# Optimization experiments

Hardware: AMD Instinct MI355X
Metric: run time of the kernel (lower is better)

The kernel has to match this reference:

```python
import jax, jax.numpy as jnp
import numpy as np

B, T, C, H = 1, 1024, 2048, 32
N = C // H  # head_dim = 64
EPS_GN = 0.00064


def setup_inputs() -> dict:
    key = jax.random.key(0)
    ks = jax.random.split(key, 40)
    f32 = jnp.float32

    def rn(k, shape, s):
        return jax.random.normal(k, shape, f32) * s

    layer_idx, n_layer = 12, 24
    r01 = layer_idx / (n_layer - 1)
    r1a0 = 1.0 - layer_idx / n_layer
    ddd = (jnp.arange(C, dtype=f32) / C).reshape(1, 1, C)
    decay_speed = -7.0 + 5.0 * (jnp.arange(C, dtype=f32) / (C - 1)) ** (0.85 + r01 ** 0.5)

    inp = dict(
        hidden_states=jax.random.normal(ks[0], (B, T, C), f32),
        Wq=rn(ks[1], (C, C), 0.02), Wk=rn(ks[2], (C, C), 0.02),
        Wv=rn(ks[3], (C, C), 0.02), Wo=rn(ks[4], (C, C), 0.02),
        time_maa_x=1.0 - ddd ** (0.6 * r1a0 ** 0.9),
        time_maa_rg=rn(ks[5], (1, 1, C), 0.01),
        time_maa_wa=rn(ks[6], (1, 1, C), 0.01),
        time_maa_k=rn(ks[7], (1, 1, C), 0.01),
        time_maa_v=rn(ks[8], (1, 1, C), 0.01),
        time_maa_w1=rn(ks[9], (C, 4 * 32), 0.01),
        time_maa_w2=rn(ks[10], (4, 32, C), 0.01),
        time_decay=decay_speed.reshape(1, 1, C) + 0.5,
        time_decay_w1=rn(ks[11], (C, 64), 0.01),
        time_decay_w2=rn(ks[12], (64, C), 0.01),
        time_aaaaa=rn(ks[13], (1, 1, C), 0.01),
        time_aaa_w1=rn(ks[14], (C, 16), 0.01),
        time_aaa_w2=rn(ks[15], (16, C), 0.01),
        time_kkk_w1=rn(ks[16], (C, 16), 0.01),
        time_kkk_w2=rn(ks[17], (16, C), 0.01),
        gate_w1=rn(ks[18], (C, 128), 0.01),
        gate_w2=rn(ks[19], (128, C), 0.01),
        time_misc_a=rn(ks[20], (1, 1, C), 0.01),
        ma_w1=rn(ks[21], (C, 16), 0.01),
        ma_w2=rn(ks[22], (16, C), 0.01),
        time_misc_k=rn(ks[23], (1, 1, C), 0.01),
        mk_w1=rn(ks[24], (C, 16), 0.01),
        mk_w2=rn(ks[25], (16, C), 0.01),
        time_faaaa=rn(ks[26], (1, 1, H, N), 0.01),
        ln_w=1.0 + rn(ks[27], (C,), 0.01),
        ln_b=rn(ks[28], (C,), 0.01),
    )
    return inp


def _wkv7(r, w, k, v, a, b):
    """RWKV7 matrix-state recurrence. Inputs [B,T,C]; per head state [N,N].
    state_t = state * exp(w_t) (per key-col) + (state @ a_t) b_t^T + v_t k_t^T;
    out_t = state_t @ r_t."""
    hs = lambda x: x.reshape(B, T, H, N)
    r, k, v, a, b = map(hs, (r, k, v, a, b))
    dec = jnp.exp(hs(w))  # w <= -0.5, decay in (0,1)

    def step(state, inp):
        r_t, d_t, k_t, v_t, a_t, b_t = inp  # each [B,H,N]
        sa = jnp.einsum('bhij,bhj->bhi', state, a_t)
        state = (state * d_t[:, :, None, :]
                 + sa[..., None] * b_t[:, :, None, :]
                 + v_t[..., None] * k_t[:, :, None, :])
        out = jnp.einsum('bhij,bhj->bhi', state, r_t)
        return state, out

    xs = tuple(jnp.moveaxis(t, 1, 0) for t in (r, dec, k, v, a, b))  # [T,B,H,N]
    state0 = jnp.zeros((B, H, N, N), r.dtype)
    _, out = jax.lax.scan(step, state0, xs)
    return jnp.moveaxis(out, 0, 1).reshape(B, T, C)


def _group_norm(x, w, b):
    xg = x.reshape(B, T, H, N)
    mu = xg.mean(-1, keepdims=True)
    var = xg.var(-1, keepdims=True)
    xn = (xg - mu) * jax.lax.rsqrt(var + EPS_GN)
    return xn.reshape(B, T, C) * w + b


def reference(hidden_states, Wq, Wk, Wv, Wo, time_maa_x, time_maa_rg, time_maa_wa,
              time_maa_k, time_maa_v, time_maa_w1, time_maa_w2, time_decay,
              time_decay_w1, time_decay_w2, time_aaaaa, time_aaa_w1, time_aaa_w2,
              time_kkk_w1, time_kkk_w2, gate_w1, gate_w2, time_misc_a, ma_w1, ma_w2,
              time_misc_k, mk_w1, mk_w2, time_faaaa, ln_w, ln_b):
    x = hidden_states  # T already multiple of 16, so no padding branch
    dxprev = jnp.pad(x, ((0, 0), (1, 0), (0, 0)))[:, :-1] - x  # token shift
    xxx = x + dxprev * time_maa_x
    mix = jnp.tanh(xxx @ time_maa_w1).reshape(B, T, 4, 32)
    mix = jnp.einsum('btfd,fdc->fbtc', mix, time_maa_w2)  # [4,B,T,C]
    mrg, mwa, mk_mix, mv = mix[0], mix[1], mix[2], mix[3]
    xrg = x + dxprev * (time_maa_rg + mrg)
    xwa = x + dxprev * (time_maa_wa + mwa)
    xk = x + dxprev * (time_maa_k + mk_mix)
    xv = x + dxprev * (time_maa_v + mv)

    r = xrg @ Wq
    w = -jax.nn.softplus(-(time_decay + jnp.tanh(xwa @ time_decay_w1) @ time_decay_w2)) - 0.5
    k = xk @ Wk
    v = xv @ Wv
    g = jnp.tanh(xrg @ gate_w1) @ gate_w2

    kk = k + jnp.tanh(xk @ time_kkk_w1) @ time_kkk_w2
    kkh = kk.reshape(B, T, H, N)
    kk = (kkh / jnp.maximum(jnp.linalg.norm(kkh, axis=-1, keepdims=True), 1e-12)).reshape(B, T, C)

    a = jax.nn.sigmoid(time_aaaaa + (xwa @ time_aaa_w1) @ time_aaa_w2)
    ma = jax.nn.sigmoid(time_misc_a + (xwa @ ma_w1) @ ma_w2)
    k = k * ma + k * a * (1.0 - ma)
    mk_g = jax.nn.sigmoid(time_misc_k + (xk @ mk_w1) @ mk_w2)
    k = k * jnp.exp(jnp.minimum(w * mk_g, 0.0))

    y = _wkv7(r, w, k, v, -kk, kk * a)
    y = _group_norm(y, ln_w, ln_b)
    rh, kh, vh = (t.reshape(B, T, H, N) for t in (r, k, v))
    y = y + ((rh * kh * time_faaaa).sum(-1, keepdims=True) * vh).reshape(B, T, C)
    return (y * g) @ Wo
```

## Files before the change

kernel.cpp:

```cpp
#include <hip/hip_runtime.h>


#define T_ 1024
#define C_ 2048
#define H_ 32
#define N_ 64

using half8  = __attribute__((ext_vector_type(8))) _Float16;
using half4  = __attribute__((ext_vector_type(4))) _Float16;
using floatx4 = __attribute__((ext_vector_type(4))) float;

#define DPP_ADD(v, ctrl) \
    ((v) + __int_as_float(__builtin_amdgcn_update_dpp( \
        0, __float_as_int(v), (ctrl), 0xf, 0xf, true)))
#define REDUCE16(v) do { \
    v = DPP_ADD(v, 0xB1); v = DPP_ADD(v, 0x4E); \
    v = DPP_ADD(v, 0x141); v = DPP_ADD(v, 0x140); } while (0)

__global__ __launch_bounds__(256) void k_tr(
    const float* __restrict__ W0, const float* __restrict__ W1,
    const float* __restrict__ W2, const float* __restrict__ W3,
    _Float16* __restrict__ D0, _Float16* __restrict__ D1,
    _Float16* __restrict__ D2, _Float16* __restrict__ D3)
{
    const int z = blockIdx.z;
    const float* S = (z == 0) ? W0 : (z == 1) ? W1 : (z == 2) ? W2 : W3;
    _Float16* D = (z == 0) ? D0 : (z == 1) ? D1 : (z == 2) ? D2 : D3;
    const int nb = blockIdx.x * 64, kb = blockIdx.y * 64;
    __shared__ __align__(16) float tile[64][65];
    const int tr = threadIdx.x >> 4, tc4 = (threadIdx.x & 15) * 4;
#pragma unroll
    for (int p = 0; p < 4; ++p) {
        int row = p * 16 + tr;
        float4 v = *(const float4*)&S[(size_t)(kb + row) * C_ + nb + tc4];
        tile[row][tc4 + 0] = v.x; tile[row][tc4 + 1] = v.y;
        tile[row][tc4 + 2] = v.z; tile[row][tc4 + 3] = v.w;
    }
    __syncthreads();
#pragma unroll
    for (int p = 0; p < 4; ++p) {
        int n = p * 16 + tr;
        half4 u;
        u[0] = (_Float16)tile[tc4 + 0][n];
        u[1] = (_Float16)tile[tc4 + 1][n];
        u[2] = (_Float16)tile[tc4 + 2][n];
        u[3] = (_Float16)tile[tc4 + 3][n];
        *(half4*)&D[(size_t)(nb + n) * C_ + kb + tc4] = u;
    }
}

__global__ __launch_bounds__(256) void k_trW(
    const float* __restrict__ maa_w1, const float* __restrict__ gate_w1,
    const float* __restrict__ decay_w1, const float* __restrict__ aaa_w1,
    const float* __restrict__ ma_w1, const float* __restrict__ kkk_w1,
    const float* __restrict__ mk_w1,
    _Float16* __restrict__ WTm, _Float16* __restrict__ WTl)
{
    const int z = blockIdx.z;
    const int k = blockIdx.x * 256 + threadIdx.x;
    const int n = blockIdx.y;
    if (z == 0 && n >= 128) return;
    const float* src; int stride, col;
    _Float16* dst;
    if (z == 0) { src = maa_w1; stride = 128; col = n; dst = WTm; }
    else {
        dst = WTl;
        if (n < 128)      { src = gate_w1;  stride = 128; col = n; }
        else if (n < 192) { src = decay_w1; stride = 64;  col = n - 128; }
        else if (n < 208) { src = aaa_w1;   stride = 16;  col = n - 192; }
        else if (n < 224) { src = ma_w1;    stride = 16;  col = n - 208; }
        else if (n < 240) { src = kkk_w1;   stride = 16;  col = n - 224; }
        else              { src = mk_w1;    stride = 16;  col = n - 240; }
    }
    dst[(size_t)n * C_ + k] = (_Float16)src[(size_t)k * stride + col];
}

__global__ __launch_bounds__(256) void k_prep(
    const float* __restrict__ X, const float* __restrict__ maa_x,
    _Float16* __restrict__ xxxH)
{
    const size_t idx = (size_t)blockIdx.x * 256 + threadIdx.x;
    const int c = (int)(idx & (C_ - 1));
    float cur = X[idx];
    float prev = (idx >= C_) ? X[idx - C_] : 0.0f;
    xxxH[idx] = (_Float16)(cur + (prev - cur) * maa_x[c]);
}

__global__ __launch_bounds__(256) void k_lora(
    int which,
    const _Float16* __restrict__ Axxx, const _Float16* __restrict__ Axrg,
    const _Float16* __restrict__ Axwa, const _Float16* __restrict__ Axk,
    const _Float16* __restrict__ WTm, const _Float16* __restrict__ WTl,
    float* __restrict__ m1p, float* __restrict__ l2p)
{
    const int mt = blockIdx.x;
    const int nt = blockIdx.y;
    const int ks = blockIdx.z;
    const _Float16* A; const _Float16* BT; float* O; int ostride;
    if (which == 0) { A = Axxx; BT = WTm; O = m1p; ostride = 128; }
    else {
        BT = WTl; O = l2p; ostride = 256;
        A = (nt < 4) ? Axrg : (nt < 7) ? Axwa : Axk;
    }
    O += (size_t)ks * T_ * ostride;
    const int m0 = mt * 64, n0 = nt * 32, k0 = ks * 512;
    const int tid = threadIdx.x;
    __shared__ __align__(16) _Float16 As[64 * 40];
    __shared__ __align__(16) _Float16 Bs[32 * 40];
    const int lane = tid & 63, wv = tid >> 6;
    const int r16 = lane & 15, q = lane >> 4;

    floatx4 acc[2];
    { floatx4 zv = {0.f, 0.f, 0.f, 0.f}; acc[0] = zv; acc[1] = zv; }

    const int arow = tid >> 2, ac8 = (tid & 3) * 8;
    const _Float16* ag = A + (size_t)(m0 + arow) * C_ + k0 + ac8;
    const _Float16* bg = BT + (size_t)(n0 + (tid >> 2)) * C_ + k0 + ac8;

    for (int kc = 0; kc < 512; kc += 32) {
        half8 av = *(const half8*)(ag + kc);
        half8 bv;
        if (tid < 128) bv = *(const half8*)(bg + kc);
        *(half8*)&As[arow * 40 + ac8] = av;
        if (tid < 128) *(half8*)&Bs[(tid >> 2) * 40 + ac8] = bv;
        __syncthreads();
        half8 af = *(const half8*)&As[(wv * 16 + r16) * 40 + q * 8];
        half8 b0 = *(const half8*)&Bs[(r16) * 40 + q * 8];
        half8 b1 = *(const half8*)&Bs[(16 + r16) * 40 + q * 8];
        acc[0] = __builtin_amdgcn_mfma_f32_16x16x32_f16(af, b0, acc[0], 0, 0, 0);
        acc[1] = __builtin_amdgcn_mfma_f32_16x16x32_f16(af, b1, acc[1], 0, 0, 0);
        __syncthreads();
    }
#pragma unroll
    for (int j = 0; j < 2; ++j)
#pragma unroll
        for (int e = 0; e < 4; ++e) {
            int row = m0 + wv * 16 + q * 4 + e;
            int col = n0 + j * 16 + r16;
            O[(size_t)row * ostride + col] = acc[j][e];
        }
}

__global__ __launch_bounds__(256) void k_xmix(
    const float* __restrict__ X, const float* __restrict__ m1p,
    const float* __restrict__ w2,
    const float* __restrict__ mrg, const float* __restrict__ mwa,
    const float* __restrict__ mk, const float* __restrict__ mv,
    _Float16* __restrict__ xrgH, _Float16* __restrict__ xwaH,
    _Float16* __restrict__ xkH, _Float16* __restrict__ xvH)
{
    const int tid = threadIdx.x;
    const int c = blockIdx.x * 256 + tid;
    const int t0 = blockIdx.y * 16;
    const size_t P = (size_t)T_ * 128;
    __shared__ __align__(16) float m1s[16][128];
#pragma unroll
    for (int p = 0; p < 2; ++p) {
        int id = tid + p * 256;
        int r = id >> 5, c4 = (id & 31) * 4;
        size_t off = (size_t)(t0 + r) * 128 + c4;
        float4 v0 = *(const float4*)&m1p[off];
        float4 v1 = *(const float4*)&m1p[P + off];
        float4 v2 = *(const float4*)&m1p[2 * P + off];
        float4 v3 = *(const float4*)&m1p[3 * P + off];
        float4 v;
        v.x = tanhf(((v0.x + v1.x) + v2.x) + v3.x);
        v.y = tanhf(((v0.y + v1.y) + v2.y) + v3.y);
        v.z = tanhf(((v0.z + v1.z) + v2.z) + v3.z);
        v.w = tanhf(((v0.w + v1.w) + v2.w) + v3.w);
        *(float4*)&m1s[r][c4] = v;
    }
    __syncthreads();
    float a0[16], a1[16], a2[16], a3[16];
#pragma unroll
    for (int t = 0; t < 16; ++t) { a0[t] = 0.f; a1[t] = 0.f; a2[t] = 0.f; a3[t] = 0.f; }
    for (int d = 0; d < 32; ++d) {
        float w0 = w2[(size_t)(0 * 32 + d) * C_ + c];
        float w1 = w2[(size_t)(1 * 32 + d) * C_ + c];
        float w2v = w2[(size_t)(2 * 32 + d) * C_ + c];
        float w3 = w2[(size_t)(3 * 32 + d) * C_ + c];
#pragma unroll
        for (int t = 0; t < 16; ++t) {
            a0[t] = fmaf(m1s[t][d],      w0,  a0[t]);
            a1[t] = fmaf(m1s[t][32 + d], w1,  a1[t]);
            a2[t] = fmaf(m1s[t][64 + d], w2v, a2[t]);
            a3[t] = fmaf(m1s[t][96 + d], w3,  a3[t]);
        }
    }
    float vrg = mrg[c], vwa = mwa[c], vmk = mk[c], vmv = mv[c];
    float prev = (t0 > 0) ? X[(size_t)(t0 - 1) * C_ + c] : 0.0f;
    for (int t = 0; t < 16; ++t) {
        size_t idx = (size_t)(t0 + t) * C_ + c;
        float cur = X[idx];
        float dx = prev - cur;
        xrgH[idx] = (_Float16)(cur + dx * (vrg + a0[t]));
        xwaH[idx] = (_Float16)(cur + dx * (vwa + a1[t]));
        xkH[idx]  = (_Float16)(cur + dx * (vmk + a2[t]));
        xvH[idx]  = (_Float16)(cur + dx * (vmv + a3[t]));
        prev = cur;
    }
}

__global__ __launch_bounds__(256) void k_gemm(
    const _Float16* __restrict__ A0, const _Float16* __restrict__ B0, float* __restrict__ C0,
    const _Float16* __restrict__ A1, const _Float16* __restrict__ B1, float* __restrict__ C1,
    const _Float16* __restrict__ A2, const _Float16* __restrict__ B2, float* __restrict__ C2)
{
    const int z = blockIdx.z;
    const _Float16* A = (z == 0) ? A0 : (z == 1) ? A1 : A2;
    const _Float16* Bt = (z == 0) ? B0 : (z == 1) ? B1 : B2;
    float* C = (z == 0) ? C0 : (z == 1) ? C1 : C2;
    const int mtile = blockIdx.y * 128;
    const int ntile = blockIdx.x * 128;
    const int tid = threadIdx.x;
    __shared__ __align__(16) _Float16 As[128 * 40];
    __shared__ __align__(16) _Float16 Bs[128 * 40];
    const int lane = tid & 63;
    const int wvid = tid >> 6;
    const int wm = wvid >> 1, wn = wvid & 1;
    const int r16 = lane & 15, q = lane >> 4;

    floatx4 acc[4][4];
#pragma unroll
    for (int i = 0; i < 4; ++i)
#pragma unroll
        for (int j = 0; j < 4; ++j) { floatx4 zv = {0.f, 0.f, 0.f, 0.f}; acc[i][j] = zv; }

    const int srow = tid >> 1, shalf = tid & 1;
    const _Float16* ag = A + (size_t)(mtile + srow) * C_ + shalf * 16;
    const _Float16* bg = Bt + (size_t)(ntile + srow) * C_ + shalf * 16;
    _Float16* asw = &As[srow * 40 + shalf * 16];
    _Float16* bsw = &Bs[srow * 40 + shalf * 16];

    for (int kc = 0; kc < C_; kc += 32) {
        half8 a0 = *(const half8*)(ag + kc);
        half8 a1 = *(const half8*)(ag + kc + 8);
        half8 b0 = *(const half8*)(bg + kc);
        half8 b1 = *(const half8*)(bg + kc + 8);
        *(half8*)asw = a0; *(half8*)(asw + 8) = a1;
        *(half8*)bsw = b0; *(half8*)(bsw + 8) = b1;
        __syncthreads();

        half8 af[4], bf[4];
#pragma unroll
        for (int i = 0; i < 4; ++i)
            af[i] = *(const half8*)&As[(wm * 64 + i * 16 + r16) * 40 + q * 8];
#pragma unroll
        for (int j = 0; j < 4; ++j)
            bf[j] = *(const half8*)&Bs[(wn * 64 + j * 16 + r16) * 40 + q * 8];
#pragma unroll
        for (int i = 0; i < 4; ++i)
#pragma unroll
            for (int j = 0; j < 4; ++j)
                acc[i][j] = __builtin_amdgcn_mfma_f32_16x16x32_f16(af[i], bf[j], acc[i][j], 0, 0, 0);
        __syncthreads();
    }
#pragma unroll
    for (int i = 0; i < 4; ++i)
#pragma unroll
        for (int j = 0; j < 4; ++j)
#pragma unroll
            for (int e = 0; e < 4; ++e) {
                int row = mtile + wm * 64 + i * 16 + q * 4 + e;
                int col = ntile + wn * 64 + j * 16 + r16;
                C[(size_t)row * C_ + col] = acc[i][j][e];
            }
}

__global__ __launch_bounds__(256) void k_fuse(
    const float* __restrict__ l2p,
    float* __restrict__ K0,
    const float* __restrict__ decay_w2, const float* __restrict__ aaa_w2,
    const float* __restrict__ ma_w2, const float* __restrict__ kkk_w2,
    const float* __restrict__ mk_w2,
    const float* __restrict__ tdecay, const float* __restrict__ aaaaa,
    const float* __restrict__ misc_a, const float* __restrict__ misc_k,
    float* __restrict__ Wout, float* __restrict__ KKout, float* __restrict__ Aout)
{
    const int tid = threadIdx.x;
    const int c = blockIdx.x * 256 + tid;
    const int t0 = blockIdx.y * 16;
    const size_t P = (size_t)T_ * 256;
    __shared__ __align__(16) float wsS[16][96];
    __shared__ __align__(16) float ksS[16][32];
    for (int id = tid; id < 16 * 24; id += 256) {
        int r = id / 24, c4 = (id % 24) * 4;
        size_t off = (size_t)(t0 + r) * 256 + 128 + c4;
        float4 v0 = *(const float4*)&l2p[off];
        float4 v1 = *(const float4*)&l2p[P + off];
        float4 v2 = *(const float4*)&l2p[2 * P + off];
        float4 v3 = *(const float4*)&l2p[3 * P + off];
        float4 v;
        v.x = ((v0.x + v1.x) + v2.x) + v3.x;
        v.y = ((v0.y + v1.y) + v2.y) + v3.y;
        v.z = ((v0.z + v1.z) + v2.z) + v3.z;
        v.w = ((v0.w + v1.w) + v2.w) + v3.w;
        if (c4 < 64) { v.x = tanhf(v.x); v.y = tanhf(v.y); v.z = tanhf(v.z); v.w = tanhf(v.w); }
        *(float4*)&wsS[r][c4] = v;
    }
    for (int id = tid; id < 16 * 8; id += 256) {
        int r = id / 8, c4 = (id % 8) * 4;
        size_t off = (size_t)(t0 + r) * 256 + 224 + c4;
        float4 v0 = *(const float4*)&l2p[off];
        float4 v1 = *(const float4*)&l2p[P + off];
        float4 v2 = *(const float4*)&l2p[2 * P + off];
        float4 v3 = *(const float4*)&l2p[3 * P + off];
        float4 v;
        v.x = ((v0.x + v1.x) + v2.x) + v3.x;
        v.y = ((v0.y + v1.y) + v2.y) + v3.y;
        v.z = ((v0.z + v1.z) + v2.z) + v3.z;
        v.w = ((v0.w + v1.w) + v2.w) + v3.w;
        if (c4 < 16) { v.x = tanhf(v.x); v.y = tanhf(v.y); v.z = tanhf(v.z); v.w = tanhf(v.w); }
        *(float4*)&ksS[r][c4] = v;
    }
    __syncthreads();
    float accW[16], accA[16], accMA[16], accKK[16], accMK[16];
#pragma unroll
    for (int r = 0; r < 16; ++r) { accW[r] = 0.f; accA[r] = 0.f; accMA[r] = 0.f; accKK[r] = 0.f; accMK[r] = 0.f; }
    for (int j = 0; j < 64; ++j) {
        float w = decay_w2[(size_t)j * C_ + c];
#pragma unroll
        for (int r = 0; r < 16; ++r) accW[r] = fmaf(wsS[r][j], w, accW[r]);
    }
    for (int j = 0; j < 16; ++j) {
        float wa = aaa_w2[(size_t)j * C_ + c];
        float wm = ma_w2[(size_t)j * C_ + c];
        float wk = kkk_w2[(size_t)j * C_ + c];
        float wq = mk_w2[(size_t)j * C_ + c];
#pragma unroll
        for (int r = 0; r < 16; ++r) {
            accA[r]  = fmaf(wsS[r][64 + j], wa, accA[r]);
            accMA[r] = fmaf(wsS[r][80 + j], wm, accMA[r]);
            accKK[r] = fmaf(ksS[r][j],      wk, accKK[r]);
            accMK[r] = fmaf(ksS[r][16 + j], wq, accMK[r]);
        }
    }
    float td = tdecay[c], aa = aaaaa[c], mia = misc_a[c], mik = misc_k[c];
    for (int r = 0; r < 16; ++r) {
        size_t idx = (size_t)(t0 + r) * C_ + c;
        float wraw = td + accW[r];
        float w = -logf(1.0f + __expf(-wraw)) - 0.5f;
        float a  = 1.0f / (1.0f + __expf(-(aa  + accA[r])));
        float mav = 1.0f / (1.0f + __expf(-(mia + accMA[r])));
        float mkv = 1.0f / (1.0f + __expf(-(mik + accMK[r])));
        float k0 = K0[idx];
        Wout[idx]  = w;
        KKout[idx] = k0 + accKK[r];
        K0[idx]    = k0 * (mav + a * (1.0f - mav)) * __expf(fminf(w * mkv, 0.0f));
        Aout[idx]  = a;
    }
}

__global__ __launch_bounds__(256) void k_kknorm(float* __restrict__ KK, float* __restrict__ Ab)
{
    const int t = blockIdx.y;
    const int c = blockIdx.x * 256 + threadIdx.x;
    const size_t idx = (size_t)t * C_ + c;
    float kv = KK[idx];
    float ss = kv * kv;
    ss += __shfl_xor(ss, 1, 64);  ss += __shfl_xor(ss, 2, 64);
    ss += __shfl_xor(ss, 4, 64);  ss += __shfl_xor(ss, 8, 64);
    ss += __shfl_xor(ss, 16, 64); ss += __shfl_xor(ss, 32, 64);
    float scale = 1.0f / fmaxf(sqrtf(ss), 1e-12f);
    float kn = kv * scale;
    KK[idx] = kn;
    Ab[idx] = kn * Ab[idx];
}

__global__ __launch_bounds__(256) void k_gate2(
    const float* __restrict__ l2p, const float* __restrict__ w2, float* __restrict__ G)
{
    const int tid = threadIdx.x;
    const int c = blockIdx.x * 256 + tid;
    const int t0 = blockIdx.y * 16;
    const size_t P = (size_t)T_ * 256;
    __shared__ __align__(16) float gs[16][128];
#pragma unroll
    for (int p = 0; p < 2; ++p) {
        int id = tid + p * 256;
        int r = id >> 5, c4 = (id & 31) * 4;
        size_t off = (size_t)(t0 + r) * 256 + c4;
        float4 v0 = *(const float4*)&l2p[off];
        float4 v1 = *(const float4*)&l2p[P + off];
        float4 v2 = *(const float4*)&l2p[2 * P + off];
        float4 v3 = *(const float4*)&l2p[3 * P + off];
        float4 v;
        v.x = tanhf(((v0.x + v1.x) + v2.x) + v3.x);
        v.y = tanhf(((v0.y + v1.y) + v2.y) + v3.y);
        v.z = tanhf(((v0.z + v1.z) + v2.z) + v3.z);
        v.w = tanhf(((v0.w + v1.w) + v2.w) + v3.w);
        *(float4*)&gs[r][c4] = v;
    }
    __syncthreads();
    float acc[16];
#pragma unroll
    for (int r = 0; r < 16; ++r) acc[r] = 0.f;
    for (int j = 0; j < 128; ++j) {
        float w = w2[(size_t)j * C_ + c];
#pragma unroll
        for (int r = 0; r < 16; ++r) acc[r] = fmaf(gs[r][j], w, acc[r]);
    }
    for (int r = 0; r < 16; ++r) G[(size_t)(t0 + r) * C_ + c] = acc[r];
}

__global__ __launch_bounds__(256) void k_wkv(
    const float* __restrict__ R, const float* __restrict__ Wd,
    const float* __restrict__ K, const float* __restrict__ V,
    const float* __restrict__ KK, const float* __restrict__ Bb,
    float* __restrict__ Y)
{
    const int tid = threadIdx.x;
    const int h = blockIdx.x >> 2;
    const int rg = blockIdx.x & 3;
    const int c0 = h * 64;
    const int wv = tid >> 6, lane = tid & 63;
    const int irow = rg * 16 + wv * 4 + (lane >> 4);
    const int jg = lane & 15;
    __shared__ __align__(16) float rS[16][64], dS[16][64], kS[16][64],
                                   vS[16][64], aS[16][64], bS[16][64], oS[16][64];
    float4 s = make_float4(0.f, 0.f, 0.f, 0.f);
    const int tloc = tid >> 4, j4 = (tid & 15) * 4;

    for (int tc = 0; tc < T_; tc += 16) {
        size_t gi = (size_t)(tc + tloc) * C_ + c0 + j4;
        *(float4*)&rS[tloc][j4] = *(const float4*)&R[gi];
        float4 w4 = *(const float4*)&Wd[gi];
        float4 d4;
        d4.x = __expf(w4.x); d4.y = __expf(w4.y); d4.z = __expf(w4.z); d4.w = __expf(w4.w);
        *(float4*)&dS[tloc][j4] = d4;
        *(float4*)&kS[tloc][j4] = *(const float4*)&K[gi];
        *(float4*)&vS[tloc][j4] = *(const float4*)&V[gi];
        float4 kk4 = *(const float4*)&KK[gi];
        float4 a4 = make_float4(-kk4.x, -kk4.y, -kk4.z, -kk4.w);
        *(float4*)&aS[tloc][j4] = a4;
        *(float4*)&bS[tloc][j4] = *(const float4*)&Bb[gi];
        __syncthreads();

#pragma unroll
        for (int tt = 0; tt < 16; ++tt) {
            float4 a = *(float4*)&aS[tt][jg * 4];
            float sa = s.x * a.x + s.y * a.y + s.z * a.z + s.w * a.w;
            REDUCE16(sa);
            float vi = vS[tt][irow];
            float4 d = *(float4*)&dS[tt][jg * 4];
            float4 b = *(float4*)&bS[tt][jg * 4];
            float4 k = *(float4*)&kS[tt][jg * 4];
            s.x = fmaf(s.x, d.x, fmaf(sa, b.x, vi * k.x));
            s.y = fmaf(s.y, d.y, fmaf(sa, b.y, vi * k.y));
            s.z = fmaf(s.z, d.z, fmaf(sa, b.z, vi * k.z));
            s.w = fmaf(s.w, d.w, fmaf(sa, b.w, vi * k.w));
            float4 r = *(float4*)&rS[tt][jg * 4];
            float o = s.x * r.x + s.y * r.y + s.z * r.z + s.w * r.w;
            REDUCE16(o);
            if (jg == 0) oS[tt][irow] = o;
        }
        __syncthreads();
        Y[(size_t)(tc + tloc) * C_ + c0 + rg * 16 + (tid & 15)] = oS[tloc][rg * 16 + (tid & 15)];
    }
}

__global__ __launch_bounds__(256) void k_gn(
    const float* __restrict__ Y, const float* __restrict__ R, const float* __restrict__ K,
    const float* __restrict__ V, const float* __restrict__ G,
    const float* __restrict__ faaaa, const float* __restrict__ lnw,
    const float* __restrict__ lnb, _Float16* __restrict__ YG)
{
    const int t = blockIdx.y;
    const int c = blockIdx.x * 256 + threadIdx.x;
    const size_t idx = (size_t)t * C_ + c;
    float y = Y[idx];
    float s1 = y, s2 = y * y;
#pragma unroll
    for (int off = 1; off < 64; off <<= 1) {
        s1 += __shfl_xor(s1, off, 64);
        s2 += __shfl_xor(s2, off, 64);
    }
    float mu = s1 * (1.0f / 64.0f);
    float var = s2 * (1.0f / 64.0f) - mu * mu;
    float gn = (y - mu) * rsqrtf(var + 0.00064f) * lnw[c] + lnb[c];
    float p = R[idx] * K[idx] * faaaa[c];
#pragma unroll
    for (int off = 1; off < 64; off <<= 1) p += __shfl_xor(p, off, 64);
    float y2 = gn + p * V[idx];
    YG[idx] = (_Float16)(y2 * G[idx]);
}

extern "C" void kernel_launch(void* const* d_in, const int* in_sizes, int n_in,
                              void* d_out, int out_size, void* d_ws, size_t ws_size,
                              hipStream_t stream)
{
    (void)in_sizes; (void)n_in; (void)out_size; (void)ws_size;
    const float* hidden   = (const float*)d_in[0];
    const float* Wq       = (const float*)d_in[1];
    const float* Wk       = (const float*)d_in[2];
    const float* Wv       = (const float*)d_in[3];
    const float* Wo       = (const float*)d_in[4];
    const float* maa_x    = (const float*)d_in[5];
    const float* maa_rg   = (const float*)d_in[6];
    const float* maa_wa   = (const float*)d_in[7];
    const float* maa_k    = (const float*)d_in[8];
    const float* maa_v    = (const float*)d_in[9];
    const float* maa_w1   = (const float*)d_in[10];
    const float* maa_w2   = (const float*)d_in[11];
    const float* tdecay   = (const float*)d_in[12];
    const float* decay_w1 = (const float*)d_in[13];
    const float* decay_w2 = (const float*)d_in[14];
    const float* aaaaa    = (const float*)d_in[15];
    const float* aaa_w1   = (const float*)d_in[16];
    const float* aaa_w2   = (const float*)d_in[17];
    const float* kkk_w1   = (const float*)d_in[18];
    const float* kkk_w2   = (const float*)d_in[19];
    const float* gate_w1  = (const float*)d_in[20];
    const float* gate_w2  = (const float*)d_in[21];
    const float* misc_a   = (const float*)d_in[22];
    const float* ma_w1    = (const float*)d_in[23];
    const float* ma_w2    = (const float*)d_in[24];
    const float* misc_k   = (const float*)d_in[25];
    const float* mk_w1    = (const float*)d_in[26];
    const float* mk_w2    = (const float*)d_in[27];
    const float* faaaa    = (const float*)d_in[28];
    const float* lnw      = (const float*)d_in[29];
    const float* lnb      = (const float*)d_in[30];

    float* ws = (float*)d_ws;
    const size_t TC = (size_t)T_ * C_;
    float* S0 = ws + 0 * TC;
    float* S1 = ws + 1 * TC;
    float* S2 = ws + 2 * TC;
    float* S3 = ws + 3 * TC;
    float* S4 = ws + 4 * TC;
    float* S5 = ws + 5 * TC;
    float* S6 = ws + 6 * TC;
    float* S7 = ws + 7 * TC;
    float* m1p = ws + 8 * TC;
    float* l2p = m1p + (size_t)4 * T_ * 128;
    _Float16* WTq = (_Float16*)(l2p + (size_t)4 * T_ * 256);
    _Float16* WTk = WTq + (size_t)C_ * C_;
    _Float16* WTv = WTk + (size_t)C_ * C_;
    _Float16* WTo = WTv + (size_t)C_ * C_;
    _Float16* WTm = WTo + (size_t)C_ * C_;
    _Float16* WTl = WTm + (size_t)128 * C_;
    _Float16* xxxH = WTl + (size_t)256 * C_;
    _Float16* xrgH = xxxH + TC;
    _Float16* xwaH = xrgH + TC;
    _Float16* xkH  = xwaH + TC;
    _Float16* xvH  = xkH + TC;
    _Float16* ygH  = xxxH;
    float* out = (float*)d_out;

    k_tr<<<dim3(32, 32, 4), 256, 0, stream>>>(Wq, Wk, Wv, Wo, WTq, WTk, WTv, WTo);
    k_trW<<<dim3(8, 256, 2), 256, 0, stream>>>(maa_w1, gate_w1, decay_w1,
        aaa_w1, ma_w1, kkk_w1, mk_w1, WTm, WTl);
    k_prep<<<dim3((int)(TC / 256)), 256, 0, stream>>>(hidden, maa_x, xxxH);
    k_lora<<<dim3(16, 4, 4), 256, 0, stream>>>(0, xxxH, xxxH, xxxH, xxxH,
        WTm, WTl, m1p, l2p);
    k_xmix<<<dim3(8, 64), 256, 0, stream>>>(hidden, m1p, maa_w2,
        maa_rg, maa_wa, maa_k, maa_v, xrgH, xwaH, xkH, xvH);
    k_lora<<<dim3(16, 8, 4), 256, 0, stream>>>(1, xxxH, xrgH, xwaH, xkH,
        WTm, WTl, m1p, l2p);
    k_gemm<<<dim3(16, 8, 3), 256, 0, stream>>>(
        xrgH, WTq, S4,  xkH, WTk, S6,  xvH, WTv, S7);
    k_fuse<<<dim3(8, 64), 256, 0, stream>>>(l2p, S6, decay_w2, aaa_w2, ma_w2,
        kkk_w2, mk_w2, tdecay, aaaaa, misc_a, misc_k, S5, S3, S2);
    k_kknorm<<<dim3(8, 1024), 256, 0, stream>>>(S3, S2);
    k_gate2<<<dim3(8, 64), 256, 0, stream>>>(l2p, gate_w2, S1);
    k_wkv<<<dim3(128), 256, 0, stream>>>(S4, S5, S6, S7, S3, S2, S0);
    k_gn<<<dim3(8, 1024), 256, 0, stream>>>(S0, S4, S6, S7, S1, faaaa, lnw, lnb, ygH);
    k_gemm<<<dim3(16, 8, 1), 256, 0, stream>>>(
        ygH, WTo, out,  ygH, WTo, out,  ygH, WTo, out);
}
```

Before: 604.5 us.

## Fuse kk-norm and gate LoRA into neighbors, async LDS loads, register-stream WKV

The kk L2 normalisation and the b=kk*a product move into k_fuse, which uses a wave reduction. The gate LoRA second stage is folded into k_gn, which recomputes tanh of the gate hidden per row and takes a 128-term dot product per element. Together these remove two kernel launches and several full T×C passes through memory. The GEMM now stages tiles with global_load_lds direct-to-LDS copies and drops the padded row stride, which may add LDS bank conflicts. The WKV kernel streams inputs through registers in chunks of 8 timesteps instead of LDS with barriers, and k_gn now does extra per-element work.

New measurement: 654.1 us. 8.2% more time.

```diff
diff --git a/kernel.cpp b/kernel.cpp
--- a/kernel.cpp
+++ b/kernel.cpp
@@ -16,6 +16,12 @@
 #define REDUCE16(v) do { \
     v = DPP_ADD(v, 0xB1); v = DPP_ADD(v, 0x4E); \
     v = DPP_ADD(v, 0x141); v = DPP_ADD(v, 0x140); } while (0)
+
+__device__ __forceinline__ void async_cp16(const _Float16* g, _Float16* l) {
+    __builtin_amdgcn_global_load_lds(
+        (const __attribute__((address_space(1))) void*)g,
+        (__attribute__((address_space(3))) void*)l, 16, 0, 0);
+}
 
 __global__ __launch_bounds__(256) void k_tr(
     const float* __restrict__ W0, const float* __restrict__ W1,
@@ -213,8 +219,8 @@
     const int mtile = blockIdx.y * 128;
     const int ntile = blockIdx.x * 128;
     const int tid = threadIdx.x;
-    __shared__ __align__(16) _Float16 As[128 * 40];
-    __shared__ __align__(16) _Float16 Bs[128 * 40];
+    __shared__ __align__(16) _Float16 As[128 * 32];
+    __shared__ __align__(16) _Float16 Bs[128 * 32];
     const int lane = tid & 63;
     const int wvid = tid >> 6;
     const int wm = wvid >> 1, wn = wvid & 1;
@@ -226,28 +232,27 @@
 #pragma unroll
         for (int j = 0; j < 4; ++j) { floatx4 zv = {0.f, 0.f, 0.f, 0.f}; acc[i][j] = zv; }
 
-    const int srow = tid >> 1, shalf = tid & 1;
-    const _Float16* ag = A + (size_t)(mtile + srow) * C_ + shalf * 16;
-    const _Float16* bg = Bt + (size_t)(ntile + srow) * C_ + shalf * 16;
-    _Float16* asw = &As[srow * 40 + shalf * 16];
-    _Float16* bsw = &Bs[srow * 40 + shalf * 16];
+    const int srow = tid >> 2, sq = tid & 3;
+    const _Float16* agA = A + (size_t)(mtile + srow) * C_ + sq * 8;
+    const _Float16* agB = Bt + (size_t)(ntile + srow) * C_ + sq * 8;
+    _Float16* ldsA = &As[srow * 32 + sq * 8];
+    _Float16* ldsB = &Bs[srow * 32 + sq * 8];
+    const size_t rowoff = (size_t)64 * C_;
 
     for (int kc = 0; kc < C_; kc += 32) {
-        half8 a0 = *(const half8*)(ag + kc);
-        half8 a1 = *(const half8*)(ag + kc + 8);
-        half8 b0 = *(const half8*)(bg + kc);
-        half8 b1 = *(const half8*)(bg + kc + 8);
-        *(half8*)asw = a0; *(half8*)(asw + 8) = a1;
-        *(half8*)bsw = b0; *(half8*)(bsw + 8) = b1;
+        async_cp16(agA + kc, ldsA);
+        async_cp16(agA + kc + rowoff, ldsA + 64 * 32);
+        async_cp16(agB + kc, ldsB);
+        async_cp16(agB + kc + rowoff, ldsB + 64 * 32);
         __syncthreads();
 
         half8 af[4], bf[4];
 #pragma unroll
         for (int i = 0; i < 4; ++i)
-            af[i] = *(const half8*)&As[(wm * 64 + i * 16 + r16) * 40 + q * 8];
+            af[i] = *(const half8*)&As[(wm * 64 + i * 16 + r16) * 32 + q * 8];
 #pragma unroll
         for (int j = 0; j < 4; ++j)
-            bf[j] = *(const half8*)&Bs[(wn * 64 + j * 16 + r16) * 40 + q * 8];
+            bf[j] = *(const half8*)&Bs[(wn * 64 + j * 16 + r16) * 32 + q * 8];
 #pragma unroll
         for (int i = 0; i < 4; ++i)
 #pragma unroll
@@ -275,7 +280,7 @@
     const float* __restrict__ mk_w2,
     const float* __restrict__ tdecay, const float* __restrict__ aaaaa,
     const float* __restrict__ misc_a, const float* __restrict__ misc_k,
-    float* __restrict__ Wout, float* __restrict__ KKout, float* __restrict__ Aout)
+    float* __restrict__ Wout, float* __restrict__ KKout, float* __restrict__ Bout)
 {
     const int tid = threadIdx.x;
     const int c = blockIdx.x * 256 + tid;
@@ -344,66 +349,20 @@
         float mav = 1.0f / (1.0f + __expf(-(mia + accMA[r])));
         float mkv = 1.0f / (1.0f + __expf(-(mik + accMK[r])));
         float k0 = K0[idx];
+        float kkun = k0 + accKK[r];
+        float ss = kkun * kkun;
+        REDUCE16(ss);
+        ss += __shfl_xor(ss, 16, 64);
+        ss += __shfl_xor(ss, 32, 64);
+        float kn = kkun * (1.0f / fmaxf(sqrtf(ss), 1e-12f));
         Wout[idx]  = w;
-        KKout[idx] = k0 + accKK[r];
+        KKout[idx] = kn;
+        Bout[idx]  = kn * a;
         K0[idx]    = k0 * (mav + a * (1.0f - mav)) * __expf(fminf(w * mkv, 0.0f));
-        Aout[idx]  = a;
-    }
-}
-
-__global__ __launch_bounds__(256) void k_kknorm(float* __restrict__ KK, float* __restrict__ Ab)
-{
-    const int t = blockIdx.y;
-    const int c = blockIdx.x * 256 + threadIdx.x;
-    const size_t idx = (size_t)t * C_ + c;
-    float kv = KK[idx];
-    float ss = kv * kv;
-    ss += __shfl_xor(ss, 1, 64);  ss += __shfl_xor(ss, 2, 64);
-    ss += __shfl_xor(ss, 4, 64);  ss += __shfl_xor(ss, 8, 64);
-    ss += __shfl_xor(ss, 16, 64); ss += __shfl_xor(ss, 32, 64);
-    float scale = 1.0f / fmaxf(sqrtf(ss), 1e-12f);
-    float kn = kv * scale;
-    KK[idx] = kn;
-    Ab[idx] = kn * Ab[idx];
-}
-
-__global__ __launch_bounds__(256) void k_gate2(
-    const float* __restrict__ l2p, const float* __restrict__ w2, float* __restrict__ G)
-{
-    const int tid = threadIdx.x;
-    const int c = blockIdx.x * 256 + tid;
-    const int t0 = blockIdx.y * 16;
-    const size_t P = (size_t)T_ * 256;
-    __shared__ __align__(16) float gs[16][128];
-#pragma unroll
-    for (int p = 0; p < 2; ++p) {
-        int id = tid + p * 256;
-        int r = id >> 5, c4 = (id & 31) * 4;
-        size_t off = (size_t)(t0 + r) * 256 + c4;
-        float4 v0 = *(const float4*)&l2p[off];
-        float4 v1 = *(const float4*)&l2p[P + off];
-        float4 v2 = *(const float4*)&l2p[2 * P + off];
-        float4 v3 = *(const float4*)&l2p[3 * P + off];
-        float4 v;
-        v.x = tanhf(((v0.x + v1.x) + v2.x) + v3.x);
-        v.y = tanhf(((v0.y + v1.y) + v2.y) + v3.y);
-        v.z = tanhf(((v0.z + v1.z) + v2.z) + v3.z);
-        v.w = tanhf(((v0.w + v1.w) + v2.w) + v3.w);
-        *(float4*)&gs[r][c4] = v;
-    }
-    __syncthreads();
-    float acc[16];
-#pragma unroll
-    for (int r = 0; r < 16; ++r) acc[r] = 0.f;
-    for (int j = 0; j < 128; ++j) {
-        float w = w2[(size_t)j * C_ + c];
-#pragma unroll
-        for (int r = 0; r < 16; ++r) acc[r] = fmaf(gs[r][j], w, acc[r]);
-    }
-    for (int r = 0; r < 16; ++r) G[(size_t)(t0 + r) * C_ + c] = acc[r];
-}
-
-__global__ __launch_bounds__(256) void k_wkv(
+    }
+}
+
+__global__ __launch_bounds__(256, 1) void k_wkv(
     const float* __restrict__ R, const float* __restrict__ Wd,
     const float* __restrict__ K, const float* __restrict__ V,
     const float* __restrict__ KK, const float* __restrict__ Bb,
@@ -416,58 +375,60 @@
     const int wv = tid >> 6, lane = tid & 63;
     const int irow = rg * 16 + wv * 4 + (lane >> 4);
     const int jg = lane & 15;
-    __shared__ __align__(16) float rS[16][64], dS[16][64], kS[16][64],
-                                   vS[16][64], aS[16][64], bS[16][64], oS[16][64];
+    const int j4 = jg * 4;
+
     float4 s = make_float4(0.f, 0.f, 0.f, 0.f);
-    const int tloc = tid >> 4, j4 = (tid & 15) * 4;
-
-    for (int tc = 0; tc < T_; tc += 16) {
-        size_t gi = (size_t)(tc + tloc) * C_ + c0 + j4;
-        *(float4*)&rS[tloc][j4] = *(const float4*)&R[gi];
-        float4 w4 = *(const float4*)&Wd[gi];
-        float4 d4;
-        d4.x = __expf(w4.x); d4.y = __expf(w4.y); d4.z = __expf(w4.z); d4.w = __expf(w4.w);
-        *(float4*)&dS[tloc][j4] = d4;
-        *(float4*)&kS[tloc][j4] = *(const float4*)&K[gi];
-        *(float4*)&vS[tloc][j4] = *(const float4*)&V[gi];
-        float4 kk4 = *(const float4*)&KK[gi];
-        float4 a4 = make_float4(-kk4.x, -kk4.y, -kk4.z, -kk4.w);
-        *(float4*)&aS[tloc][j4] = a4;
-        *(float4*)&bS[tloc][j4] = *(const float4*)&Bb[gi];
-        __syncthreads();
-
-#pragma unroll
-        for (int tt = 0; tt < 16; ++tt) {
-            float4 a = *(float4*)&aS[tt][jg * 4];
-            float sa = s.x * a.x + s.y * a.y + s.z * a.z + s.w * a.w;
+
+    for (int tc = 0; tc < T_; tc += 8) {
+        float4 rr[8], ww[8], kq[8], aq[8], bq[8];
+        float vv[8];
+#pragma unroll
+        for (int u = 0; u < 8; ++u) {
+            const size_t base = (size_t)(tc + u) * C_ + c0;
+            rr[u] = *(const float4*)&R[base + j4];
+            ww[u] = *(const float4*)&Wd[base + j4];
+            kq[u] = *(const float4*)&K[base + j4];
+            aq[u] = *(const float4*)&KK[base + j4];
+            bq[u] = *(const float4*)&Bb[base + j4];
+            vv[u] = V[base + irow];
+        }
+#pragma unroll
+        for (int u = 0; u < 8; ++u) {
+            float4 d;
+            d.x = __expf(ww[u].x); d.y = __expf(ww[u].y);
+            d.z = __expf(ww[u].z); d.w = __expf(ww[u].w);
+            float sa = -(s.x * aq[u].x + s.y * aq[u].y + s.z * aq[u].z + s.w * aq[u].w);
             REDUCE16(sa);
-            float vi = vS[tt][irow];
-            float4 d = *(float4*)&dS[tt][jg * 4];
-            float4 b = *(float4*)&bS[tt][jg * 4];
-            float4 k = *(float4*)&kS[tt][jg * 4];
-            s.x = fmaf(s.x, d.x, fmaf(sa, b.x, vi * k.x));
-            s.y = fmaf(s.y, d.y, fmaf(sa, b.y, vi * k.y));
-            s.z = fmaf(s.z, d.z, fmaf(sa, b.z, vi * k.z));
-            s.w = fmaf(s.w, d.w, fmaf(sa, b.w, vi * k.w));
-            float4 r = *(float4*)&rS[tt][jg * 4];
-            float o = s.x * r.x + s.y * r.y + s.z * r.z + s.w * r.w;
+            float vi = vv[u];
+            s.x = fmaf(s.x, d.x, fmaf(sa, bq[u].x, vi * kq[u].x));
+            s.y = fmaf(s.y, d.y, fmaf(sa, bq[u].y, vi * kq[u].y));
+            s.z = fmaf(s.z, d.z, fmaf(sa, bq[u].z, vi * kq[u].z));
+            s.w = fmaf(s.w, d.w, fmaf(sa, bq[u].w, vi * kq[u].w));
+            float o = s.x * rr[u].x + s.y * rr[u].y + s.z * rr[u].z + s.w * rr[u].w;
             REDUCE16(o);
-            if (jg == 0) oS[tt][irow] = o;
+            if (jg == 0) Y[(size_t)(tc + u) * C_ + c0 + irow] = o;
         }
-        __syncthreads();
-        Y[(size_t)(tc + tloc) * C_ + c0 + rg * 16 + (tid & 15)] = oS[tloc][rg * 16 + (tid & 15)];
     }
 }
 
 __global__ __launch_bounds__(256) void k_gn(
     const float* __restrict__ Y, const float* __restrict__ R, const float* __restrict__ K,
-    const float* __restrict__ V, const float* __restrict__ G,
+    const float* __restrict__ V, const float* __restrict__ l2p,
+    const float* __restrict__ gw2,
     const float* __restrict__ faaaa, const float* __restrict__ lnw,
     const float* __restrict__ lnb, _Float16* __restrict__ YG)
 {
     const int t = blockIdx.y;
     const int c = blockIdx.x * 256 + threadIdx.x;
     const size_t idx = (size_t)t * C_ + c;
+    __shared__ __align__(16) float gs[128];
+    if (threadIdx.x < 128) {
+        const size_t P = (size_t)T_ * 256;
+        size_t off = (size_t)t * 256 + threadIdx.x;
+        float v = ((l2p[off] + l2p[P + off]) + l2p[2 * P + off]) + l2p[3 * P + off];
+        gs[threadIdx.x] = tanhf(v);
+    }
+    __syncthreads();
     float y = Y[idx];
     float s1 = y, s2 = y * y;
 #pragma unroll
@@ -482,7 +443,9 @@
 #pragma unroll
     for (int off = 1; off < 64; off <<= 1) p += __shfl_xor(p, off, 64);
     float y2 = gn + p * V[idx];
-    YG[idx] = (_Float16)(y2 * G[idx]);
+    float g = 0.f;
+    for (int j = 0; j < 128; ++j) g = fmaf(gs[j], gw2[(size_t)j * C_ + c], g);
+    YG[idx] = (_Float16)(y2 * g);
 }
 
 extern "C" void kernel_launch(void* const* d_in, const int* in_sizes, int n_in,
@@ -525,7 +488,6 @@
     float* ws = (float*)d_ws;
     const size_t TC = (size_t)T_ * C_;
     float* S0 = ws + 0 * TC;
-    float* S1 = ws + 1 * TC;
     float* S2 = ws + 2 * TC;
     float* S3 = ws + 3 * TC;
     float* S4 = ws + 4 * TC;
@@ -562,10 +524,9 @@
         xrgH, WTq, S4,  xkH, WTk, S6,  xvH, WTv, S7);
     k_fuse<<<dim3(8, 64), 256, 0, stream>>>(l2p, S6, decay_w2, aaa_w2, ma_w2,
         kkk_w2, mk_w2, tdecay, aaaaa, misc_a, misc_k, S5, S3, S2);
-    k_kknorm<<<dim3(8, 1024), 256, 0, stream>>>(S3, S2);
-    k_gate2<<<dim3(8, 64), 256, 0, stream>>>(l2p, gate_w2, S1);
     k_wkv<<<dim3(128), 256, 0, stream>>>(S4, S5, S6, S7, S3, S2, S0);
-    k_gn<<<dim3(8, 1024), 256, 0, stream>>>(S0, S4, S6, S7, S1, faaaa, lnw, lnb, ygH);
+    k_gn<<<dim3(8, 1024), 256, 0, stream>>>(S0, S4, S6, S7, l2p, gate_w2,
+        faaaa, lnw, lnb, ygH);
     k_gemm<<<dim3(16, 8, 1), 256, 0, stream>>>(
         ygH, WTo, out,  ygH, WTo, out,  ygH, WTo, out);
 }
```
